# Kernel tuning notes

Measured on AMD Instinct MI355X. Metric: run time of the kernel, lower is better.

## Reference

```python
import jax, jax.numpy as jnp
import numpy as np

N_PATCH = 8      # patch_num = [8, 8]
N_BINS = 256     # histogram bins 0..255


def setup_inputs() -> dict:
    key = jax.random.key(0)
    k1, k2 = jax.random.split(key)
    sr = jax.random.uniform(k1, (16, 3, 1024, 1024), dtype=jnp.float32)
    hr = jax.random.uniform(k2, (16, 3, 1024, 1024), dtype=jnp.float32)
    return {"sr": sr, "hr": hr}


def _entropy_weight(hr):
    """Per-spatial-patch Shannon entropy of 8-bit histogram, broadcast to an
    [H, W] weight map, normalized as (w - w.min()) / w.max() (original w.max,
    matching torch evaluation order)."""
    B, C, H, W = hr.shape
    ph, pw = H // N_PATCH, W // N_PATCH
    # [64, B*C*ph*pw] — each patch covers the full batch+channel slice,
    # exactly as split_patch's img[..., i*ph:(i+1)*ph, j*pw:(j+1)*pw].
    patches = (hr.reshape(B, C, N_PATCH, ph, N_PATCH, pw)
                 .transpose(2, 4, 0, 1, 3, 5)
                 .reshape(N_PATCH * N_PATCH, -1))
    # (patch * 255).int() truncation; values in [0,1) -> bins 0..255
    vals = jnp.clip((patches * 255.0).astype(jnp.int32), 0, N_BINS - 1)
    counts = jax.vmap(lambda v: jnp.bincount(v, length=N_BINS))(vals)
    p = counts.astype(jnp.float32) / jnp.float32(vals.shape[1])  # density (unit bin width)
    safe_p = jnp.where(p > 0, p, 1.0)
    ent = -jnp.sum(jnp.where(p > 0, p * jnp.log2(safe_p), 0.0), axis=1)  # [64]
    # tile each patch's scalar entropy over its spatial block (row-major patch order)
    w = jnp.broadcast_to(ent.reshape(N_PATCH, 1, N_PATCH, 1),
                         (N_PATCH, ph, N_PATCH, pw)).reshape(H, W)
    w = (w - w.min()) / w.max()
    return w  # [H, W], broadcasts over B, C


def reference(sr, hr):
    w = _entropy_weight(hr)
    # L1 loss (mean reduction) on entropy-weighted images
    return jnp.mean(jnp.abs(w * sr - w * hr))
```

## Files before the change

kernel.cpp:

```cpp
#include <hip/hip_runtime.h>
#include <math.h>

#define NP      8
#define NBINS   256
#define BC      48
#define HH      1024
#define WW      1024
#define ROWS_PER_BLOCK 32
#define THREADS 256
#define NBLOCKS 1536
#define PATCH_ELEMS (BC * 128 * 128)
#define N_TOTAL ((long long)BC * HH * WW)

__global__ __launch_bounds__(THREADS)
void entrop_pass1(const float* __restrict__ sr, const float* __restrict__ hr,
                  unsigned int* __restrict__ ghist, float* __restrict__ gsum)
{
    __shared__ unsigned int hist[NP * NBINS];
    const int t = threadIdx.x;
    for (int m = t; m < NP * NBINS; m += THREADS) hist[m] = 0;
    __syncthreads();

    const long long r0 = (long long)blockIdx.x * ROWS_PER_BLOCK;
    const int h0 = (int)(r0 & (HH - 1));
    const int i  = h0 >> 7;
    const int j  = t >> 5;

    const float4* s4 = (const float4*)sr + r0 * (WW / 4);
    const float4* h4 = (const float4*)hr + r0 * (WW / 4);

    float acc = 0.0f;
    #pragma unroll 4
    for (int r = 0; r < ROWS_PER_BLOCK; ++r) {
        const int idx = r * (WW / 4) + t;
        float4 s = s4[idx];
        float4 h = h4[idx];

        acc += fabsf(s.x - h.x);
        acc += fabsf(s.y - h.y);
        acc += fabsf(s.z - h.z);
        acc += fabsf(s.w - h.w);

        int b0 = (int)(h.x * 255.0f); b0 = min(max(b0, 0), 255);
        int b1 = (int)(h.y * 255.0f); b1 = min(max(b1, 0), 255);
        int b2 = (int)(h.z * 255.0f); b2 = min(max(b2, 0), 255);
        int b3 = (int)(h.w * 255.0f); b3 = min(max(b3, 0), 255);
        atomicAdd(&hist[(j << 8) + b0], 1u);
        atomicAdd(&hist[(j << 8) + b1], 1u);
        atomicAdd(&hist[(j << 8) + b2], 1u);
        atomicAdd(&hist[(j << 8) + b3], 1u);
    }

    for (int off = 16; off; off >>= 1) acc += __shfl_down(acc, off, 32);
    if ((t & 31) == 0) atomicAdd(&gsum[i * NP + j], acc);

    __syncthreads();
    for (int m = t; m < NP * NBINS; m += THREADS) {
        unsigned int c = hist[m];
        if (c) atomicAdd(&ghist[(i * NP * NBINS) + m], c);
    }
}

__global__ __launch_bounds__(THREADS)
void entrop_pass2(const unsigned int* __restrict__ ghist,
                  const float* __restrict__ gsum,
                  float* __restrict__ out)
{
    __shared__ double red[THREADS / 64];
    __shared__ double ent[NP * NP];
    const int t = threadIdx.x;
    const double inv_n = 1.0 / (double)PATCH_ELEMS;

    for (int p = 0; p < NP * NP; ++p) {
        unsigned int c = ghist[p * NBINS + t];
        double term = 0.0;
        if (c) {
            double pd = (double)c * inv_n;
            term = pd * log2(pd);
        }
        for (int off = 32; off; off >>= 1) term += __shfl_down(term, off, 64);
        if ((t & 63) == 0) red[t >> 6] = term;
        __syncthreads();
        if (t == 0) ent[p] = -(red[0] + red[1] + red[2] + red[3]);
        __syncthreads();
    }

    if (t == 0) {
        double mn = ent[0], mx = ent[0];
        for (int p = 1; p < NP * NP; ++p) {
            mn = fmin(mn, ent[p]);
            mx = fmax(mx, ent[p]);
        }
        double total = 0.0;
        for (int p = 0; p < NP * NP; ++p) {
            double w = (ent[p] - mn) / mx;
            total += w * (double)gsum[p];
        }
        out[0] = (float)(total / (double)N_TOTAL);
    }
}

extern "C" void kernel_launch(void* const* d_in, const int* in_sizes, int n_in,
                              void* d_out, int out_size, void* d_ws, size_t ws_size,
                              hipStream_t stream)
{
    const float* sr = (const float*)d_in[0];
    const float* hr = (const float*)d_in[1];
    float* out = (float*)d_out;

    unsigned int* ghist = (unsigned int*)d_ws;
    float* gsum = (float*)((char*)d_ws + NP * NP * NBINS * sizeof(unsigned int));

    const size_t zero_bytes = NP * NP * NBINS * sizeof(unsigned int)
                            + NP * NP * sizeof(float);
    hipMemsetAsync(d_ws, 0, zero_bytes, stream);

    entrop_pass1<<<NBLOCKS, THREADS, 0, stream>>>(sr, hr, ghist, gsum);
    entrop_pass2<<<1, THREADS, 0, stream>>>(ghist, gsum, out);
}
```

Before: 471.0 us.

## Replace global atomics with per-block 16-bit histogram partials and parallel reduction

Pass 1 now uses 16-row blocks (twice as many blocks) with double-buffered register loads. When workspace is large enough, each block writes its shared histogram packed as 16-bit counts and its partial sums to its own slot instead of doing global atomics, which also removes the memset. A 64-block reduction kernel then sums the partials and computes entropies in parallel, and a single-wave final kernel does the min/max and weighted sum with shuffles. This trades global atomic contention and a serial single-block tail for extra workspace traffic (about 12 MB of partials) and an additional launch; a fallback atomic path is kept for small workspaces.

Result: faster. 405.5 us (-13.9%).

```diff
diff --git a/kernel.cpp b/kernel.cpp
--- a/kernel.cpp
+++ b/kernel.cpp
@@ -6,98 +6,178 @@
 #define BC      48
 #define HH      1024
 #define WW      1024
-#define ROWS_PER_BLOCK 32
+#define RPB     16
 #define THREADS 256
-#define NBLOCKS 1536
+#define NBLK1   3072
+#define BLK_PER_I 384
 #define PATCH_ELEMS (BC * 128 * 128)
 #define N_TOTAL ((long long)BC * HH * WW)
 
-__global__ __launch_bounds__(THREADS)
-void entrop_pass1(const float* __restrict__ sr, const float* __restrict__ hr,
-                  unsigned int* __restrict__ ghist, float* __restrict__ gsum)
-{
-    __shared__ unsigned int hist[NP * NBINS];
-    const int t = threadIdx.x;
-    for (int m = t; m < NP * NBINS; m += THREADS) hist[m] = 0;
-    __syncthreads();
-
-    const long long r0 = (long long)blockIdx.x * ROWS_PER_BLOCK;
-    const int h0 = (int)(r0 & (HH - 1));
-    const int i  = h0 >> 7;
-    const int j  = t >> 5;
-
-    const float4* s4 = (const float4*)sr + r0 * (WW / 4);
-    const float4* h4 = (const float4*)hr + r0 * (WW / 4);
-
-    float acc = 0.0f;
-    #pragma unroll 4
-    for (int r = 0; r < ROWS_PER_BLOCK; ++r) {
-        const int idx = r * (WW / 4) + t;
-        float4 s = s4[idx];
-        float4 h = h4[idx];
-
+#define GH_BYTES   ((size_t)NBLK1 * 2048 * 2)
+#define GS_OFF     GH_BYTES
+#define GS_BYTES   ((size_t)NBLK1 * NP * 4)
+#define ENT_OFF    (GS_OFF + GS_BYTES)
+#define ENT_BYTES  (64 * 8)
+#define GT_OFF     (ENT_OFF + ENT_BYTES)
+#define PATHA_BYTES (GT_OFF + 64 * 4)
+#define B_GHIST_BYTES (64 * NBINS * 4)
+#define B_GSUM_OFF    B_GHIST_BYTES
+#define B_ENT_OFF     (B_GSUM_OFF + 256)
+
+__device__ __forceinline__ void load_g(const float4* __restrict__ s4,
+                                       const float4* __restrict__ h4,
+                                       int g, float4* sb, float4* hb)
+{
+#pragma unroll
+    for (int k = 0; k < 2; ++k) {
+        sb[k] = s4[(g * 2 + k) * (WW / 4)];
+        hb[k] = h4[(g * 2 + k) * (WW / 4)];
+    }
+}
+
+__device__ __forceinline__ void proc_g(const float4* sb, const float4* hb,
+                                       float& acc, unsigned int* histj)
+{
+#pragma unroll
+    for (int k = 0; k < 2; ++k) {
+        float4 s = sb[k], h = hb[k];
         acc += fabsf(s.x - h.x);
         acc += fabsf(s.y - h.y);
         acc += fabsf(s.z - h.z);
         acc += fabsf(s.w - h.w);
-
-        int b0 = (int)(h.x * 255.0f); b0 = min(max(b0, 0), 255);
-        int b1 = (int)(h.y * 255.0f); b1 = min(max(b1, 0), 255);
-        int b2 = (int)(h.z * 255.0f); b2 = min(max(b2, 0), 255);
-        int b3 = (int)(h.w * 255.0f); b3 = min(max(b3, 0), 255);
-        atomicAdd(&hist[(j << 8) + b0], 1u);
-        atomicAdd(&hist[(j << 8) + b1], 1u);
-        atomicAdd(&hist[(j << 8) + b2], 1u);
-        atomicAdd(&hist[(j << 8) + b3], 1u);
-    }
+        int b0 = min(max((int)(h.x * 255.0f), 0), 255);
+        int b1 = min(max((int)(h.y * 255.0f), 0), 255);
+        int b2 = min(max((int)(h.z * 255.0f), 0), 255);
+        int b3 = min(max((int)(h.w * 255.0f), 0), 255);
+        atomicAdd(&histj[b0], 1u);
+        atomicAdd(&histj[b1], 1u);
+        atomicAdd(&histj[b2], 1u);
+        atomicAdd(&histj[b3], 1u);
+    }
+}
+
+template <bool ATOMIC>
+__global__ __launch_bounds__(THREADS, 8)
+void entrop_pass1(const float* __restrict__ sr, const float* __restrict__ hr,
+                  unsigned int* __restrict__ gh32, float* __restrict__ gs)
+{
+    __shared__ unsigned int hist[NP * NBINS];
+    const int t = threadIdx.x;
+#pragma unroll
+    for (int m = t; m < NP * NBINS; m += THREADS) hist[m] = 0;
+    __syncthreads();
+
+    const int r0 = blockIdx.x * RPB;
+    const int i  = (r0 & (HH - 1)) >> 7;
+    const int j  = t >> 5;
+    unsigned int* histj = &hist[j << 8];
+
+    const float4* s4 = (const float4*)sr + (size_t)r0 * (WW / 4) + t;
+    const float4* h4 = (const float4*)hr + (size_t)r0 * (WW / 4) + t;
+
+    float acc = 0.0f;
+    float4 sA[2], hA[2], sB[2], hB[2];
+    load_g(s4, h4, 0, sA, hA);
+#pragma unroll
+    for (int g = 0; g < 7; ++g) {
+        if (g & 1) { load_g(s4, h4, g + 1, sA, hA); proc_g(sB, hB, acc, histj); }
+        else       { load_g(s4, h4, g + 1, sB, hB); proc_g(sA, hA, acc, histj); }
+    }
+    proc_g(sB, hB, acc, histj);
 
     for (int off = 16; off; off >>= 1) acc += __shfl_down(acc, off, 32);
-    if ((t & 31) == 0) atomicAdd(&gsum[i * NP + j], acc);
-
-    __syncthreads();
-    for (int m = t; m < NP * NBINS; m += THREADS) {
-        unsigned int c = hist[m];
-        if (c) atomicAdd(&ghist[(i * NP * NBINS) + m], c);
+    if ((t & 31) == 0) {
+        if (ATOMIC) atomicAdd(&gs[i * NP + j], acc);
+        else        gs[blockIdx.x * NP + j] = acc;
+    }
+
+    __syncthreads();
+    if (ATOMIC) {
+        for (int m = t; m < NP * NBINS; m += THREADS) {
+            unsigned int c = hist[m];
+            if (c) atomicAdd(&gh32[i * NP * NBINS + m], c);
+        }
+    } else {
+#pragma unroll
+        for (int m = t; m < NP * NBINS / 2; m += THREADS)
+            gh32[(size_t)blockIdx.x * (NP * NBINS / 2) + m] =
+                hist[2 * m] | (hist[2 * m + 1] << 16);
     }
 }
 
 __global__ __launch_bounds__(THREADS)
-void entrop_pass2(const unsigned int* __restrict__ ghist,
-                  const float* __restrict__ gsum,
-                  float* __restrict__ out)
-{
-    __shared__ double red[THREADS / 64];
-    __shared__ double ent[NP * NP];
+void entrop_reduceA(const unsigned short* __restrict__ gh,
+                    const float* __restrict__ gs,
+                    double* __restrict__ ent, float* __restrict__ gsumT)
+{
+    const int p = blockIdx.x, i = p >> 3, jj = p & 7;
     const int t = threadIdx.x;
-    const double inv_n = 1.0 / (double)PATCH_ELEMS;
-
-    for (int p = 0; p < NP * NP; ++p) {
-        unsigned int c = ghist[p * NBINS + t];
-        double term = 0.0;
-        if (c) {
-            double pd = (double)c * inv_n;
-            term = pd * log2(pd);
-        }
-        for (int off = 32; off; off >>= 1) term += __shfl_down(term, off, 64);
-        if ((t & 63) == 0) red[t >> 6] = term;
-        __syncthreads();
-        if (t == 0) ent[p] = -(red[0] + red[1] + red[2] + red[3]);
-        __syncthreads();
-    }
-
+
+    unsigned int cnt = 0;
+    const unsigned short* col = gh + jj * NBINS + t;
+    for (int g = 0; g < BLK_PER_I / 8; ++g) {
+#pragma unroll
+        for (int d = 0; d < 8; ++d)
+            cnt += col[(size_t)(64 * g + 8 * i + d) * 2048];
+    }
+    double term = 0.0;
+    if (cnt) {
+        double pd = (double)cnt * (1.0 / (double)PATCH_ELEMS);
+        term = pd * log2(pd);
+    }
+    float sg = 0.0f;
+    for (int idx = t; idx < BLK_PER_I; idx += THREADS) {
+        int g = idx >> 3, d = idx & 7;
+        sg += gs[(size_t)(64 * g + 8 * i + d) * NP + jj];
+    }
+
+    for (int off = 32; off; off >>= 1) {
+        term += __shfl_down(term, off, 64);
+        sg   += __shfl_down(sg, off, 64);
+    }
+    __shared__ double rd[4];
+    __shared__ float  rf[4];
+    if ((t & 63) == 0) { rd[t >> 6] = term; rf[t >> 6] = sg; }
+    __syncthreads();
     if (t == 0) {
-        double mn = ent[0], mx = ent[0];
-        for (int p = 1; p < NP * NP; ++p) {
-            mn = fmin(mn, ent[p]);
-            mx = fmax(mx, ent[p]);
-        }
-        double total = 0.0;
-        for (int p = 0; p < NP * NP; ++p) {
-            double w = (ent[p] - mn) / mx;
-            total += w * (double)gsum[p];
-        }
-        out[0] = (float)(total / (double)N_TOTAL);
-    }
+        ent[p]   = -(rd[0] + rd[1] + rd[2] + rd[3]);
+        gsumT[p] = rf[0] + rf[1] + rf[2] + rf[3];
+    }
+}
+
+__global__ __launch_bounds__(THREADS)
+void entrop_reduceB(const unsigned int* __restrict__ ghist, double* __restrict__ ent)
+{
+    const int p = blockIdx.x, t = threadIdx.x;
+    unsigned int c = ghist[p * NBINS + t];
+    double term = 0.0;
+    if (c) {
+        double pd = (double)c * (1.0 / (double)PATCH_ELEMS);
+        term = pd * log2(pd);
+    }
+    for (int off = 32; off; off >>= 1) term += __shfl_down(term, off, 64);
+    __shared__ double rd[4];
+    if ((t & 63) == 0) rd[t >> 6] = term;
+    __syncthreads();
+    if (t == 0) ent[p] = -(rd[0] + rd[1] + rd[2] + rd[3]);
+}
+
+__global__ void entrop_final(const double* __restrict__ ent,
+                             const float* __restrict__ gsumT,
+                             float* __restrict__ out)
+{
+    const int t = threadIdx.x;
+    double e = ent[t];
+    double mn = e, mx = e;
+#pragma unroll
+    for (int off = 32; off; off >>= 1) {
+        mn = fmin(mn, __shfl_xor(mn, off, 64));
+        mx = fmax(mx, __shfl_xor(mx, off, 64));
+    }
+    double contrib = (e - mn) / mx * (double)gsumT[t];
+#pragma unroll
+    for (int off = 32; off; off >>= 1) contrib += __shfl_xor(contrib, off, 64);
+    if (t == 0) out[0] = (float)(contrib / (double)N_TOTAL);
 }
 
 extern "C" void kernel_launch(void* const* d_in, const int* in_sizes, int n_in,
@@ -107,14 +187,23 @@
     const float* sr = (const float*)d_in[0];
     const float* hr = (const float*)d_in[1];
     float* out = (float*)d_out;
-
-    unsigned int* ghist = (unsigned int*)d_ws;
-    float* gsum = (float*)((char*)d_ws + NP * NP * NBINS * sizeof(unsigned int));
-
-    const size_t zero_bytes = NP * NP * NBINS * sizeof(unsigned int)
-                            + NP * NP * sizeof(float);
-    hipMemsetAsync(d_ws, 0, zero_bytes, stream);
-
-    entrop_pass1<<<NBLOCKS, THREADS, 0, stream>>>(sr, hr, ghist, gsum);
-    entrop_pass2<<<1, THREADS, 0, stream>>>(ghist, gsum, out);
-}
+    char* ws = (char*)d_ws;
+
+    if (ws_size >= PATHA_BYTES) {
+        unsigned int*   gh32  = (unsigned int*)ws;
+        float*          gs    = (float*)(ws + GS_OFF);
+        double*         ent   = (double*)(ws + ENT_OFF);
+        float*          gsumT = (float*)(ws + GT_OFF);
+        entrop_pass1<false><<<NBLK1, THREADS, 0, stream>>>(sr, hr, gh32, gs);
+        entrop_reduceA<<<64, THREADS, 0, stream>>>((const unsigned short*)gh32, gs, ent, gsumT);
+        entrop_final<<<1, 64, 0, stream>>>(ent, gsumT, out);
+    } else {
+        unsigned int* ghist = (unsigned int*)ws;
+        float*        gsum  = (float*)(ws + B_GSUM_OFF);
+        double*       ent   = (double*)(ws + B_ENT_OFF);
+        hipMemsetAsync(ws, 0, B_GSUM_OFF + 256, stream);
+        entrop_pass1<true><<<NBLK1, THREADS, 0, stream>>>(sr, hr, ghist, gsum);
+        entrop_reduceB<<<64, THREADS, 0, stream>>>(ghist, ent);
+        entrop_final<<<1, 64, 0, stream>>>(ent, gsum, out);
+    }
+}
```
